# Kernel optimization log

Hardware: AMD Instinct MI355X
Metric: run time of the kernel (lower is better)

The kernel has to match this reference:

```python
import jax, jax.numpy as jnp
import numpy as np

B, T, D = 1, 1024, 2048
F_DIM = 1408
E = 8
TOPK = 2


def setup_inputs() -> dict:
    key = jax.random.key(0)
    ks = jax.random.split(key, 5)
    x = jax.random.normal(ks[0], (B, T, D), dtype=jnp.float32)
    # torch nn.Linear weight layout: [out_features, in_features]
    gate_w = jax.random.normal(ks[1], (E, D), dtype=jnp.float32) * 0.02
    gate_proj = jax.random.normal(ks[2], (E, F_DIM, D), dtype=jnp.float32) * 0.02
    up_proj = jax.random.normal(ks[3], (E, F_DIM, D), dtype=jnp.float32) * 0.02
    down_proj = jax.random.normal(ks[4], (E, D, F_DIM), dtype=jnp.float32) * 0.02
    return {"x": x, "gate_w": gate_w, "gate_proj": gate_proj,
            "up_proj": up_proj, "down_proj": down_proj}


def reference(x, gate_w, gate_proj, up_proj, down_proj):
    b, t, d = x.shape
    x_flat = x.reshape(-1, d)                                  # [N, D]
    n = x_flat.shape[0]
    # Router: top-k logits then softmax over the selected k.
    router_logits = x_flat @ gate_w.T                          # [N, E]
    top_w, sel = jax.lax.top_k(router_logits, TOPK)            # [N, K]
    top_w = jax.nn.softmax(top_w, axis=-1)                     # [N, K]
    # Scatter routing weights into dense per-token expert weights [N, E].
    tok_ids = jnp.arange(n)[:, None]
    tw = jnp.zeros((n, E), dtype=x.dtype).at[tok_ids, sel].add(top_w)
    # Dense expert compute (mathematically identical: unselected experts get
    # zero combine weight). SwiGLU per expert.
    g = jnp.einsum('nd,efd->enf', x_flat, gate_proj)           # [E, N, F]
    u = jnp.einsum('nd,efd->enf', x_flat, up_proj)             # [E, N, F]
    h = jax.nn.silu(g) * u                                     # [E, N, F]
    eo = jnp.einsum('enf,edf->end', h, down_proj)              # [E, N, D]
    out = jnp.einsum('end,ne->nd', eo, tw)                     # [N, D]
    return out.reshape(b, t, d)
```

## Files before the change

kernel.cpp:

```cpp
#include <hip/hip_runtime.h>
#include <stdint.h>

typedef __attribute__((ext_vector_type(8))) short short8;
typedef __attribute__((ext_vector_type(4))) float f32x4;
typedef unsigned int u32;
typedef unsigned short u16;

static constexpr int N_TOK = 1024;
static constexpr int DDIM = 2048;
static constexpr int FDIM = 1408;
static constexpr int NEXP = 8;
static constexpr int MAXROWS = 3072;
static constexpr int MAXTILES = 24;

static constexpr size_t O_META    = 0;
static constexpr size_t O_TEXP    = 256;
static constexpr size_t O_TROW    = 512;
static constexpr size_t O_ROWTOK  = 768;
static constexpr size_t O_TOKROWS = O_ROWTOK + (size_t)MAXROWS * 4;
static constexpr size_t O_SEL     = O_TOKROWS + 2048 * 4;
static constexpr size_t O_W       = O_SEL + 2048 * 4;
static constexpr size_t O_G       = (O_W + 2048 * 4 + 255) & ~(size_t)255;
static constexpr size_t O_U       = O_G + (size_t)MAXROWS * FDIM * 2;
static constexpr size_t O_EO      = O_U + (size_t)MAXROWS * FDIM * 2;

static __device__ __forceinline__ u16 f2bf(float f) {
    u32 u = __builtin_bit_cast(u32, f);
    u += 0x7fffu + ((u >> 16) & 1u);
    return (u16)(u >> 16);
}
static __device__ __forceinline__ float bf2f(u16 s) {
    u32 u = ((u32)s) << 16;
    return __builtin_bit_cast(float, u);
}
static __device__ __forceinline__ u32 pack2(float a, float b) {
    return (u32)f2bf(a) | ((u32)f2bf(b) << 16);
}

__global__ __launch_bounds__(256) void router_kernel(
    const float* __restrict__ x, const float* __restrict__ gw,
    int* __restrict__ sel, float* __restrict__ wout)
{
    __shared__ float xs[DDIM];
    __shared__ float lg[NEXP];
    const int tok = blockIdx.x;
    const float* xr = x + (size_t)tok * DDIM;
    for (int i = threadIdx.x; i < DDIM / 4; i += 256)
        ((float4*)xs)[i] = ((const float4*)xr)[i];
    __syncthreads();
    const int wid = threadIdx.x >> 6, lane = threadIdx.x & 63;
    for (int i = 0; i < 2; i++) {
        const int e = wid * 2 + i;
        const float* g = gw + (size_t)e * DDIM;
        float s = 0.f;
        for (int k = lane; k < DDIM; k += 64) s += xs[k] * g[k];
        for (int off = 32; off > 0; off >>= 1) s += __shfl_down(s, off);
        if (lane == 0) lg[e] = s;
    }
    __syncthreads();
    if (threadIdx.x == 0) {
        int i1 = 0;
        for (int e = 1; e < NEXP; e++) if (lg[e] > lg[i1]) i1 = e;
        int i2 = -1;
        for (int e = 0; e < NEXP; e++) {
            if (e == i1) continue;
            if (i2 < 0 || lg[e] > lg[i2]) i2 = e;
        }
        const float e2 = __expf(lg[i2] - lg[i1]);
        const float w1 = 1.f / (1.f + e2);
        sel[tok * 2] = i1; sel[tok * 2 + 1] = i2;
        wout[tok * 2] = w1; wout[tok * 2 + 1] = e2 * w1;
    }
}

__global__ __launch_bounds__(512) void build_kernel(
    const int* __restrict__ sel, const float* __restrict__ w,
    int* __restrict__ meta, int* __restrict__ tile_e, int* __restrict__ tile_r0,
    int* __restrict__ row_tok, int* __restrict__ tok_rows)
{
    __shared__ int s0[N_TOK], s1[N_TOK];
    __shared__ u16 p0[N_TOK], p1[N_TOK];
    __shared__ int counts[NEXP], offs[NEXP];
    for (int i = threadIdx.x; i < N_TOK; i += 512) {
        s0[i] = sel[i * 2]; s1[i] = sel[i * 2 + 1];
    }
    __syncthreads();
    const int e = threadIdx.x >> 6, lane = threadIdx.x & 63;
    int base = 0;
    for (int c = 0; c < N_TOK / 64; c++) {
        const int tk = c * 64 + lane;
        const int slot = (s0[tk] == e) ? 0 : ((s1[tk] == e) ? 1 : -1);
        const unsigned long long m = __ballot(slot >= 0);
        const int pre = __popcll(m & ((1ull << lane) - 1ull));
        if (slot == 0) p0[tk] = (u16)(base + pre);
        else if (slot == 1) p1[tk] = (u16)(base + pre);
        base += __popcll(m);
    }
    if (lane == 0) counts[e] = base;
    __syncthreads();
    if (threadIdx.x == 0) {
        int off = 0, nt = 0;
        for (int q = 0; q < NEXP; q++) {
            offs[q] = off;
            const int pc = (counts[q] + 127) & ~127;
            for (int i = 0; i < pc / 128; i++) { tile_e[nt] = q; tile_r0[nt] = off + i * 128; nt++; }
            off += pc;
        }
        meta[0] = nt; meta[1] = off;
    }
    __syncthreads();
    const int off = offs[e];
    for (int c = 0; c < N_TOK / 64; c++) {
        const int tk = c * 64 + lane;
        const int slot = (s0[tk] == e) ? 0 : ((s1[tk] == e) ? 1 : -1);
        if (slot >= 0) {
            const int row = off + (slot ? p1[tk] : p0[tk]);
            row_tok[row] = tk;
            tok_rows[tk * 2 + slot] = row;
        }
    }
    const int cnt = counts[e];
    const int pc = (cnt + 127) & ~127;
    for (int p = cnt + lane; p < pc; p += 64) row_tok[off + p] = -1;
}

template<bool A_BF16, int KDIM, int NDIM, bool C_F32, bool DUAL>
__global__ __launch_bounds__(512) void gemm_kernel(
    const void* __restrict__ Asrc,
    const float* __restrict__ B0all, const float* __restrict__ B1all,
    void* __restrict__ C0, void* __restrict__ C1,
    const int* __restrict__ meta, const int* __restrict__ tile_e,
    const int* __restrict__ tile_r0, const int* __restrict__ row_tok)
{
    if ((int)blockIdx.y >= meta[0]) return;
    int nb = blockIdx.x;
    const float* Ball = B0all;
    void* Cout = C0;
    if (DUAL && nb >= NDIM / 128) { nb -= NDIM / 128; Ball = B1all; Cout = C1; }
    const int n0 = nb * 128;
    const int e = tile_e[blockIdx.y];
    const int r0g = tile_r0[blockIdx.y];
    const float* B = Ball + (size_t)e * NDIM * KDIM;

    __shared__ __align__(16) u16 As[2][128 * 64];
    __shared__ __align__(16) u16 Bs[2][128 * 64];

    const int t = threadIdx.x;
    const int r16 = t >> 4, c4 = t & 15;
    const int r8 = t >> 3, g8 = t & 7;

    const float* arow_f[4]; bool avalid[4]; const u16* arow_h[2];
    if constexpr (A_BF16) {
        for (int i = 0; i < 2; i++)
            arow_h[i] = (const u16*)Asrc + (size_t)(r0g + r8 + 64 * i) * KDIM + g8 * 8;
        for (int i = 0; i < 4; i++) { arow_f[i] = nullptr; avalid[i] = true; }
    } else {
        for (int i = 0; i < 4; i++) {
            const int tok = row_tok[r0g + r16 + 32 * i];
            avalid[i] = (tok >= 0);
            arow_f[i] = (const float*)Asrc + (size_t)(tok < 0 ? 0 : tok) * KDIM + c4 * 4;
        }
        for (int i = 0; i < 2; i++) arow_h[i] = nullptr;
    }
    const float* brow[4];
    for (int i = 0; i < 4; i++)
        brow[i] = B + (size_t)(n0 + r16 + 32 * i) * KDIM + c4 * 4;

    int sOff_f[4], sOffA_h[2];
    for (int i = 0; i < 4; i++) {
        const int row = r16 + 32 * i;
        sOff_f[i] = row * 64 + (((c4 >> 1) ^ (row & 7)) * 8) + (c4 & 1) * 4;
    }
    if constexpr (A_BF16) {
        for (int i = 0; i < 2; i++) {
            const int row = r8 + 64 * i;
            sOffA_h[i] = row * 64 + ((g8 ^ (row & 7)) * 8);
        }
    }

    const int wid = t >> 6, lane = t & 63;
    const int wm = (wid >> 2) * 64, wn = (wid & 3) * 32;
    const int lr = lane & 15, lhi = lane >> 4;

    f32x4 acc[4][2];
    for (int m = 0; m < 4; m++)
        for (int n = 0; n < 2; n++)
            acc[m][n] = f32x4{0.f, 0.f, 0.f, 0.f};

    float4 pa[4], pb[4]; uint4 pah[2];

    auto LOAD = [&](int k0) {
        if constexpr (A_BF16) {
            #pragma unroll
            for (int i = 0; i < 2; i++) pah[i] = *(const uint4*)(arow_h[i] + k0);
        } else {
            #pragma unroll
            for (int i = 0; i < 4; i++)
                pa[i] = avalid[i] ? *(const float4*)(arow_f[i] + k0)
                                  : make_float4(0.f, 0.f, 0.f, 0.f);
        }
        #pragma unroll
        for (int i = 0; i < 4; i++) pb[i] = *(const float4*)(brow[i] + k0);
    };
    auto STORE = [&](int bsel) {
        if constexpr (A_BF16) {
            #pragma unroll
            for (int i = 0; i < 2; i++) *(uint4*)(&As[bsel][sOffA_h[i]]) = pah[i];
        } else {
            #pragma unroll
            for (int i = 0; i < 4; i++) {
                uint2 v; v.x = pack2(pa[i].x, pa[i].y); v.y = pack2(pa[i].z, pa[i].w);
                *(uint2*)(&As[bsel][sOff_f[i]]) = v;
            }
        }
        #pragma unroll
        for (int i = 0; i < 4; i++) {
            uint2 v; v.x = pack2(pb[i].x, pb[i].y); v.y = pack2(pb[i].z, pb[i].w);
            *(uint2*)(&Bs[bsel][sOff_f[i]]) = v;
        }
    };
    auto COMPUTE = [&](int bsel) {
        #pragma unroll
        for (int ks = 0; ks < 2; ks++) {
            short8 a[4], b[2];
            #pragma unroll
            for (int m = 0; m < 4; m++) {
                const int row = wm + m * 16 + lr;
                const int gr = (ks * 4 + lhi) ^ (row & 7);
                a[m] = *(const short8*)(&As[bsel][row * 64 + gr * 8]);
            }
            #pragma unroll
            for (int n = 0; n < 2; n++) {
                const int row = wn + n * 16 + lr;
                const int gr = (ks * 4 + lhi) ^ (row & 7);
                b[n] = *(const short8*)(&Bs[bsel][row * 64 + gr * 8]);
            }
            #pragma unroll
            for (int m = 0; m < 4; m++)
                #pragma unroll
                for (int n = 0; n < 2; n++)
                    acc[m][n] = __builtin_amdgcn_mfma_f32_16x16x32_bf16(a[m], b[n], acc[m][n], 0, 0, 0);
        }
    };

    constexpr int NT = KDIM / 64;
    LOAD(0); STORE(0);
    __syncthreads();
    for (int kt = 0; kt < NT; kt++) {
        const int cur = kt & 1;
        if (kt + 1 < NT) LOAD((kt + 1) * 64);
        COMPUTE(cur);
        if (kt + 1 < NT) {
            STORE(cur ^ 1);
            __syncthreads();
        }
    }

    for (int m = 0; m < 4; m++) {
        const int rowb = r0g + wm + m * 16 + lhi * 4;
        for (int n = 0; n < 2; n++) {
            const int col = n0 + wn + n * 16 + lr;
            const f32x4 v = acc[m][n];
            if constexpr (C_F32) {
                float* C = (float*)Cout;
                for (int j = 0; j < 4; j++) C[(size_t)(rowb + j) * NDIM + col] = v[j];
            } else {
                u16* C = (u16*)Cout;
                for (int j = 0; j < 4; j++) C[(size_t)(rowb + j) * NDIM + col] = f2bf(v[j]);
            }
        }
    }
}

__global__ __launch_bounds__(256) void swiglu_kernel(
    u16* __restrict__ g, const u16* __restrict__ u, const int* __restrict__ meta)
{
    const long total = (long)meta[0] * 128 * FDIM;
    const long idx = ((long)blockIdx.x * 256 + threadIdx.x) * 8;
    if (idx >= total) return;
    const uint4 gv = *(const uint4*)(g + idx);
    const uint4 uv = *(const uint4*)(u + idx);
    u32 gs[4] = {gv.x, gv.y, gv.z, gv.w};
    u32 us[4] = {uv.x, uv.y, uv.z, uv.w};
    u32 rs[4];
    for (int i = 0; i < 4; i++) {
        const float g0 = bf2f((u16)(gs[i] & 0xffff)), g1 = bf2f((u16)(gs[i] >> 16));
        const float u0 = bf2f((u16)(us[i] & 0xffff)), u1 = bf2f((u16)(us[i] >> 16));
        const float h0 = g0 / (1.f + __expf(-g0)) * u0;
        const float h1 = g1 / (1.f + __expf(-g1)) * u1;
        rs[i] = pack2(h0, h1);
    }
    uint4 r; r.x = rs[0]; r.y = rs[1]; r.z = rs[2]; r.w = rs[3];
    *(uint4*)(g + idx) = r;
}

__global__ __launch_bounds__(256) void combine_kernel(
    const float* __restrict__ eo, const int* __restrict__ tok_rows,
    const float* __restrict__ w, float* __restrict__ out)
{
    const int tok = blockIdx.x;
    const int r1 = tok_rows[tok * 2], r2 = tok_rows[tok * 2 + 1];
    const float w1 = w[tok * 2], w2 = w[tok * 2 + 1];
    const int d = threadIdx.x * 8;
    const float4* p1 = (const float4*)(eo + (size_t)r1 * DDIM + d);
    const float4* p2 = (const float4*)(eo + (size_t)r2 * DDIM + d);
    float4* po = (float4*)(out + (size_t)tok * DDIM + d);
    for (int i = 0; i < 2; i++) {
        const float4 a = p1[i], b = p2[i];
        float4 r;
        r.x = w1 * a.x + w2 * b.x; r.y = w1 * a.y + w2 * b.y;
        r.z = w1 * a.z + w2 * b.z; r.w = w1 * a.w + w2 * b.w;
        po[i] = r;
    }
}

extern "C" void kernel_launch(void* const* d_in, const int* in_sizes, int n_in,
                              void* d_out, int out_size, void* d_ws, size_t ws_size,
                              hipStream_t stream) {
    const float* x  = (const float*)d_in[0];
    const float* gw = (const float*)d_in[1];
    const float* gp = (const float*)d_in[2];
    const float* up = (const float*)d_in[3];
    const float* dp = (const float*)d_in[4];
    float* out = (float*)d_out;
    char* ws = (char*)d_ws;

    int*   meta     = (int*)(ws + O_META);
    int*   tile_e   = (int*)(ws + O_TEXP);
    int*   tile_r0  = (int*)(ws + O_TROW);
    int*   row_tok  = (int*)(ws + O_ROWTOK);
    int*   tok_rows = (int*)(ws + O_TOKROWS);
    int*   sel      = (int*)(ws + O_SEL);
    float* w        = (float*)(ws + O_W);
    u16*   g        = (u16*)(ws + O_G);
    u16*   u        = (u16*)(ws + O_U);
    float* eo       = (float*)(ws + O_EO);

    router_kernel<<<N_TOK, 256, 0, stream>>>(x, gw, sel, w);
    build_kernel<<<1, 512, 0, stream>>>(sel, w, meta, tile_e, tile_r0, row_tok, tok_rows);
    gemm_kernel<false, DDIM, FDIM, false, true>
        <<<dim3(2 * (FDIM / 128), MAXTILES), 512, 0, stream>>>(
            x, gp, up, g, u, meta, tile_e, tile_r0, row_tok);
    swiglu_kernel<<<(MAXROWS * FDIM) / (256 * 8), 256, 0, stream>>>(g, u, meta);
    gemm_kernel<true, FDIM, DDIM, true, false>
        <<<dim3(DDIM / 128, MAXTILES), 512, 0, stream>>>(
            g, dp, nullptr, eo, nullptr, meta, tile_e, tile_r0, row_tok);
    combine_kernel<<<N_TOK, 256, 0, stream>>>(eo, tok_rows, w, out);
}
```

Before: 196.4 us.

## Fuse gate/up GEMMs with SwiGLU epilogue, add XCD remap and register double-buffering

The gate and up projection GEMMs now run in one block that loads the A tile once and feeds two MFMA accumulator sets, applying SiLU(g)*u in the epilogue. This removes the separate SwiGLU kernel and the bf16 g/u round-trip through memory. Block indices are remapped so neighbouring tiles land on the same XCD, and the K loop is unrolled by two with two register prefetch sets. In exchange, the fused kernel uses more registers and LDS and launches half as many blocks, which may lower occupancy.

```diff
diff --git a/kernel.cpp b/kernel.cpp
--- a/kernel.cpp
+++ b/kernel.cpp
@@ -20,9 +20,8 @@
 static constexpr size_t O_TOKROWS = O_ROWTOK + (size_t)MAXROWS * 4;
 static constexpr size_t O_SEL     = O_TOKROWS + 2048 * 4;
 static constexpr size_t O_W       = O_SEL + 2048 * 4;
-static constexpr size_t O_G       = (O_W + 2048 * 4 + 255) & ~(size_t)255;
-static constexpr size_t O_U       = O_G + (size_t)MAXROWS * FDIM * 2;
-static constexpr size_t O_EO      = O_U + (size_t)MAXROWS * FDIM * 2;
+static constexpr size_t O_H       = (O_W + 2048 * 4 + 255) & ~(size_t)255;
+static constexpr size_t O_EO      = O_H + (size_t)MAXROWS * FDIM * 2;
 
 static __device__ __forceinline__ u16 f2bf(float f) {
     u32 u = __builtin_bit_cast(u32, f);
@@ -35,6 +34,14 @@
 }
 static __device__ __forceinline__ u32 pack2(float a, float b) {
     return (u32)f2bf(a) | ((u32)f2bf(b) << 16);
+}
+
+static __device__ __forceinline__ int xcd_remap_flat() {
+    const int nwg = gridDim.x * gridDim.y;
+    const int orig = blockIdx.y * gridDim.x + blockIdx.x;
+    const int q = nwg >> 3, r = nwg & 7;
+    const int xcd = orig & 7, idx = orig >> 3;
+    return (xcd < r ? xcd * (q + 1) : r * (q + 1) + (xcd - r) * q) + idx;
 }
 
 __global__ __launch_bounds__(256) void router_kernel(
@@ -74,7 +81,7 @@
 }
 
 __global__ __launch_bounds__(512) void build_kernel(
-    const int* __restrict__ sel, const float* __restrict__ w,
+    const int* __restrict__ sel,
     int* __restrict__ meta, int* __restrict__ tile_e, int* __restrict__ tile_r0,
     int* __restrict__ row_tok, int* __restrict__ tok_rows)
 {
@@ -124,26 +131,24 @@
     for (int p = cnt + lane; p < pc; p += 64) row_tok[off + p] = -1;
 }
 
-template<bool A_BF16, int KDIM, int NDIM, bool C_F32, bool DUAL>
+template<int NMAT, bool A_BF16, int KDIM, int NDIM, bool C_F32>
 __global__ __launch_bounds__(512) void gemm_kernel(
     const void* __restrict__ Asrc,
     const float* __restrict__ B0all, const float* __restrict__ B1all,
-    void* __restrict__ C0, void* __restrict__ C1,
+    void* __restrict__ Cout,
     const int* __restrict__ meta, const int* __restrict__ tile_e,
     const int* __restrict__ tile_r0, const int* __restrict__ row_tok)
 {
-    if ((int)blockIdx.y >= meta[0]) return;
-    int nb = blockIdx.x;
-    const float* Ball = B0all;
-    void* Cout = C0;
-    if (DUAL && nb >= NDIM / 128) { nb -= NDIM / 128; Ball = B1all; Cout = C1; }
+    const int flat = xcd_remap_flat();
+    const int tile = flat / gridDim.x;
+    const int nb = flat % gridDim.x;
+    if (tile >= meta[0]) return;
     const int n0 = nb * 128;
-    const int e = tile_e[blockIdx.y];
-    const int r0g = tile_r0[blockIdx.y];
-    const float* B = Ball + (size_t)e * NDIM * KDIM;
+    const int e = tile_e[tile];
+    const int r0g = tile_r0[tile];
 
     __shared__ __align__(16) u16 As[2][128 * 64];
-    __shared__ __align__(16) u16 Bs[2][128 * 64];
+    __shared__ __align__(16) u16 Bs[NMAT][2][128 * 64];
 
     const int t = threadIdx.x;
     const int r16 = t >> 4, c4 = t & 15;
@@ -151,27 +156,42 @@
 
     const float* arow_f[4]; bool avalid[4]; const u16* arow_h[2];
     if constexpr (A_BF16) {
+        #pragma unroll
         for (int i = 0; i < 2; i++)
             arow_h[i] = (const u16*)Asrc + (size_t)(r0g + r8 + 64 * i) * KDIM + g8 * 8;
         for (int i = 0; i < 4; i++) { arow_f[i] = nullptr; avalid[i] = true; }
     } else {
+        #pragma unroll
         for (int i = 0; i < 4; i++) {
             const int tok = row_tok[r0g + r16 + 32 * i];
             avalid[i] = (tok >= 0);
             arow_f[i] = (const float*)Asrc + (size_t)(tok < 0 ? 0 : tok) * KDIM + c4 * 4;
         }
-        for (int i = 0; i < 2; i++) arow_h[i] = nullptr;
-    }
-    const float* brow[4];
-    for (int i = 0; i < 4; i++)
-        brow[i] = B + (size_t)(n0 + r16 + 32 * i) * KDIM + c4 * 4;
+        arow_h[0] = arow_h[1] = nullptr;
+    }
+    const float* brow0[4];
+    const float* brow1[4];
+    {
+        const float* B0 = B0all + (size_t)e * NDIM * KDIM;
+        #pragma unroll
+        for (int i = 0; i < 4; i++)
+            brow0[i] = B0 + (size_t)(n0 + r16 + 32 * i) * KDIM + c4 * 4;
+        if constexpr (NMAT == 2) {
+            const float* B1 = B1all + (size_t)e * NDIM * KDIM;
+            #pragma unroll
+            for (int i = 0; i < 4; i++)
+                brow1[i] = B1 + (size_t)(n0 + r16 + 32 * i) * KDIM + c4 * 4;
+        }
+    }
 
     int sOff_f[4], sOffA_h[2];
+    #pragma unroll
     for (int i = 0; i < 4; i++) {
         const int row = r16 + 32 * i;
         sOff_f[i] = row * 64 + (((c4 >> 1) ^ (row & 7)) * 8) + (c4 & 1) * 4;
     }
     if constexpr (A_BF16) {
+        #pragma unroll
         for (int i = 0; i < 2; i++) {
             const int row = r8 + 64 * i;
             sOffA_h[i] = row * 64 + ((g8 ^ (row & 7)) * 8);
@@ -182,47 +202,104 @@
     const int wm = (wid >> 2) * 64, wn = (wid & 3) * 32;
     const int lr = lane & 15, lhi = lane >> 4;
 
-    f32x4 acc[4][2];
+    f32x4 acc0[4][2], acc1[4][2];
+    #pragma unroll
     for (int m = 0; m < 4; m++)
-        for (int n = 0; n < 2; n++)
-            acc[m][n] = f32x4{0.f, 0.f, 0.f, 0.f};
-
-    float4 pa[4], pb[4]; uint4 pah[2];
-
-    auto LOAD = [&](int k0) {
+        #pragma unroll
+        for (int n = 0; n < 2; n++) {
+            acc0[m][n] = f32x4{0.f, 0.f, 0.f, 0.f};
+            acc1[m][n] = f32x4{0.f, 0.f, 0.f, 0.f};
+        }
+
+    float4 paA[4], pb0A[4], pb1A[4]; uint4 pahA[2];
+    float4 paB[4], pb0B[4], pb1B[4]; uint4 pahB[2];
+
+    auto LOADA = [&](int k0) {
         if constexpr (A_BF16) {
             #pragma unroll
-            for (int i = 0; i < 2; i++) pah[i] = *(const uint4*)(arow_h[i] + k0);
+            for (int i = 0; i < 2; i++) pahA[i] = *(const uint4*)(arow_h[i] + k0);
         } else {
             #pragma unroll
             for (int i = 0; i < 4; i++)
-                pa[i] = avalid[i] ? *(const float4*)(arow_f[i] + k0)
-                                  : make_float4(0.f, 0.f, 0.f, 0.f);
-        }
-        #pragma unroll
-        for (int i = 0; i < 4; i++) pb[i] = *(const float4*)(brow[i] + k0);
+                paA[i] = avalid[i] ? *(const float4*)(arow_f[i] + k0)
+                                   : make_float4(0.f, 0.f, 0.f, 0.f);
+        }
+        #pragma unroll
+        for (int i = 0; i < 4; i++) pb0A[i] = *(const float4*)(brow0[i] + k0);
+        if constexpr (NMAT == 2) {
+            #pragma unroll
+            for (int i = 0; i < 4; i++) pb1A[i] = *(const float4*)(brow1[i] + k0);
+        }
     };
-    auto STORE = [&](int bsel) {
+    auto LOADB = [&](int k0) {
         if constexpr (A_BF16) {
             #pragma unroll
-            for (int i = 0; i < 2; i++) *(uint4*)(&As[bsel][sOffA_h[i]]) = pah[i];
+            for (int i = 0; i < 2; i++) pahB[i] = *(const uint4*)(arow_h[i] + k0);
         } else {
             #pragma unroll
+            for (int i = 0; i < 4; i++)
+                paB[i] = avalid[i] ? *(const float4*)(arow_f[i] + k0)
+                                   : make_float4(0.f, 0.f, 0.f, 0.f);
+        }
+        #pragma unroll
+        for (int i = 0; i < 4; i++) pb0B[i] = *(const float4*)(brow0[i] + k0);
+        if constexpr (NMAT == 2) {
+            #pragma unroll
+            for (int i = 0; i < 4; i++) pb1B[i] = *(const float4*)(brow1[i] + k0);
+        }
+    };
+    auto STOREA = [&](int bsel) {
+        if constexpr (A_BF16) {
+            #pragma unroll
+            for (int i = 0; i < 2; i++) *(uint4*)(&As[bsel][sOffA_h[i]]) = pahA[i];
+        } else {
+            #pragma unroll
             for (int i = 0; i < 4; i++) {
-                uint2 v; v.x = pack2(pa[i].x, pa[i].y); v.y = pack2(pa[i].z, pa[i].w);
+                uint2 v; v.x = pack2(paA[i].x, paA[i].y); v.y = pack2(paA[i].z, paA[i].w);
                 *(uint2*)(&As[bsel][sOff_f[i]]) = v;
             }
         }
         #pragma unroll
         for (int i = 0; i < 4; i++) {
-            uint2 v; v.x = pack2(pb[i].x, pb[i].y); v.y = pack2(pb[i].z, pb[i].w);
-            *(uint2*)(&Bs[bsel][sOff_f[i]]) = v;
+            uint2 v; v.x = pack2(pb0A[i].x, pb0A[i].y); v.y = pack2(pb0A[i].z, pb0A[i].w);
+            *(uint2*)(&Bs[0][bsel][sOff_f[i]]) = v;
+        }
+        if constexpr (NMAT == 2) {
+            #pragma unroll
+            for (int i = 0; i < 4; i++) {
+                uint2 v; v.x = pack2(pb1A[i].x, pb1A[i].y); v.y = pack2(pb1A[i].z, pb1A[i].w);
+                *(uint2*)(&Bs[1][bsel][sOff_f[i]]) = v;
+            }
+        }
+    };
+    auto STOREB = [&](int bsel) {
+        if constexpr (A_BF16) {
+            #pragma unroll
+            for (int i = 0; i < 2; i++) *(uint4*)(&As[bsel][sOffA_h[i]]) = pahB[i];
+        } else {
+            #pragma unroll
+            for (int i = 0; i < 4; i++) {
+                uint2 v; v.x = pack2(paB[i].x, paB[i].y); v.y = pack2(paB[i].z, paB[i].w);
+                *(uint2*)(&As[bsel][sOff_f[i]]) = v;
+            }
+        }
+        #pragma unroll
+        for (int i = 0; i < 4; i++) {
+            uint2 v; v.x = pack2(pb0B[i].x, pb0B[i].y); v.y = pack2(pb0B[i].z, pb0B[i].w);
+            *(uint2*)(&Bs[0][bsel][sOff_f[i]]) = v;
+        }
+        if constexpr (NMAT == 2) {
+            #pragma unroll
+            for (int i = 0; i < 4; i++) {
+                uint2 v; v.x = pack2(pb1B[i].x, pb1B[i].y); v.y = pack2(pb1B[i].z, pb1B[i].w);
+                *(uint2*)(&Bs[1][bsel][sOff_f[i]]) = v;
+            }
         }
     };
     auto COMPUTE = [&](int bsel) {
         #pragma unroll
         for (int ks = 0; ks < 2; ks++) {
-            short8 a[4], b[2];
+            short8 a[4], b0[2], b1[2];
             #pragma unroll
             for (int m = 0; m < 4; m++) {
                 const int row = wm + m * 16 + lr;
@@ -233,65 +310,57 @@
             for (int n = 0; n < 2; n++) {
                 const int row = wn + n * 16 + lr;
                 const int gr = (ks * 4 + lhi) ^ (row & 7);
-                b[n] = *(const short8*)(&Bs[bsel][row * 64 + gr * 8]);
+                b0[n] = *(const short8*)(&Bs[0][bsel][row * 64 + gr * 8]);
+                if constexpr (NMAT == 2)
+                    b1[n] = *(const short8*)(&Bs[1][bsel][row * 64 + gr * 8]);
             }
             #pragma unroll
             for (int m = 0; m < 4; m++)
                 #pragma unroll
-                for (int n = 0; n < 2; n++)
-                    acc[m][n] = __builtin_amdgcn_mfma_f32_16x16x32_bf16(a[m], b[n], acc[m][n], 0, 0, 0);
+                for (int n = 0; n < 2; n++) {
+                    acc0[m][n] = __builtin_amdgcn_mfma_f32_16x16x32_bf16(a[m], b0[n], acc0[m][n], 0, 0, 0);
+                    if constexpr (NMAT == 2)
+                        acc1[m][n] = __builtin_amdgcn_mfma_f32_16x16x32_bf16(a[m], b1[n], acc1[m][n], 0, 0, 0);
+                }
         }
     };
 
     constexpr int NT = KDIM / 64;
-    LOAD(0); STORE(0);
-    __syncthreads();
-    for (int kt = 0; kt < NT; kt++) {
-        const int cur = kt & 1;
-        if (kt + 1 < NT) LOAD((kt + 1) * 64);
-        COMPUTE(cur);
-        if (kt + 1 < NT) {
-            STORE(cur ^ 1);
+    LOADA(0); STOREA(0); LOADB(64);
+    __syncthreads();
+    for (int kt = 0; kt < NT; kt += 2) {
+        if (kt + 2 < NT) LOADA((kt + 2) * 64);
+        COMPUTE(0);
+        STOREB(1);
+        __syncthreads();
+        if (kt + 3 < NT) LOADB((kt + 3) * 64);
+        COMPUTE(1);
+        if (kt + 2 < NT) {
+            STOREA(0);
             __syncthreads();
         }
     }
 
+    #pragma unroll
     for (int m = 0; m < 4; m++) {
         const int rowb = r0g + wm + m * 16 + lhi * 4;
+        #pragma unroll
         for (int n = 0; n < 2; n++) {
             const int col = n0 + wn + n * 16 + lr;
-            const f32x4 v = acc[m][n];
-            if constexpr (C_F32) {
-                float* C = (float*)Cout;
-                for (int j = 0; j < 4; j++) C[(size_t)(rowb + j) * NDIM + col] = v[j];
-            } else {
-                u16* C = (u16*)Cout;
-                for (int j = 0; j < 4; j++) C[(size_t)(rowb + j) * NDIM + col] = f2bf(v[j]);
-            }
-        }
-    }
-}
-
-__global__ __launch_bounds__(256) void swiglu_kernel(
-    u16* __restrict__ g, const u16* __restrict__ u, const int* __restrict__ meta)
-{
-    const long total = (long)meta[0] * 128 * FDIM;
-    const long idx = ((long)blockIdx.x * 256 + threadIdx.x) * 8;
-    if (idx >= total) return;
-    const uint4 gv = *(const uint4*)(g + idx);
-    const uint4 uv = *(const uint4*)(u + idx);
-    u32 gs[4] = {gv.x, gv.y, gv.z, gv.w};
-    u32 us[4] = {uv.x, uv.y, uv.z, uv.w};
-    u32 rs[4];
-    for (int i = 0; i < 4; i++) {
-        const float g0 = bf2f((u16)(gs[i] & 0xffff)), g1 = bf2f((u16)(gs[i] >> 16));
-        const float u0 = bf2f((u16)(us[i] & 0xffff)), u1 = bf2f((u16)(us[i] >> 16));
-        const float h0 = g0 / (1.f + __expf(-g0)) * u0;
-        const float h1 = g1 / (1.f + __expf(-g1)) * u1;
-        rs[i] = pack2(h0, h1);
-    }
-    uint4 r; r.x = rs[0]; r.y = rs[1]; r.z = rs[2]; r.w = rs[3];
-    *(uint4*)(g + idx) = r;
+            #pragma unroll
+            for (int j = 0; j < 4; j++) {
+                if constexpr (NMAT == 2) {
+                    const float g = acc0[m][n][j], u = acc1[m][n][j];
+                    const float h = g / (1.f + __expf(-g)) * u;
+                    ((u16*)Cout)[(size_t)(rowb + j) * NDIM + col] = f2bf(h);
+                } else if constexpr (C_F32) {
+                    ((float*)Cout)[(size_t)(rowb + j) * NDIM + col] = acc0[m][n][j];
+                } else {
+                    ((u16*)Cout)[(size_t)(rowb + j) * NDIM + col] = f2bf(acc0[m][n][j]);
+                }
+            }
+        }
+    }
 }
 
 __global__ __launch_bounds__(256) void combine_kernel(
@@ -332,18 +401,16 @@
     int*   tok_rows = (int*)(ws + O_TOKROWS);
     int*   sel      = (int*)(ws + O_SEL);
     float* w        = (float*)(ws + O_W);
-    u16*   g        = (u16*)(ws + O_G);
-    u16*   u        = (u16*)(ws + O_U);
+    u16*   h        = (u16*)(ws + O_H);
     float* eo       = (float*)(ws + O_EO);
 
     router_kernel<<<N_TOK, 256, 0, stream>>>(x, gw, sel, w);
-    build_kernel<<<1, 512, 0, stream>>>(sel, w, meta, tile_e, tile_r0, row_tok, tok_rows);
-    gemm_kernel<false, DDIM, FDIM, false, true>
-        <<<dim3(2 * (FDIM / 128), MAXTILES), 512, 0, stream>>>(
-            x, gp, up, g, u, meta, tile_e, tile_r0, row_tok);
-    swiglu_kernel<<<(MAXROWS * FDIM) / (256 * 8), 256, 0, stream>>>(g, u, meta);
-    gemm_kernel<true, FDIM, DDIM, true, false>
+    build_kernel<<<1, 512, 0, stream>>>(sel, meta, tile_e, tile_r0, row_tok, tok_rows);
+    gemm_kernel<2, false, DDIM, FDIM, false>
+        <<<dim3(FDIM / 128, MAXTILES), 512, 0, stream>>>(
+            x, gp, up, h, meta, tile_e, tile_r0, row_tok);
+    gemm_kernel<1, true, FDIM, DDIM, true>
         <<<dim3(DDIM / 128, MAXTILES), 512, 0, stream>>>(
-            g, dp, nullptr, eo, nullptr, meta, tile_e, tile_r0, row_tok);
+            h, dp, nullptr, eo, meta, tile_e, tile_r0, row_tok);
     combine_kernel<<<N_TOK, 256, 0, stream>>>(eo, tok_rows, w, out);
 }
```

After: 636.1 us. 3.24x slower.
